# Performance work log

Hardware: AMD Instinct MI355X
Metric: run time of the kernel (lower is better)

## Reference

```python
import jax, jax.numpy as jnp
import numpy as np

NEG_INF = -1.0e12  # matches masked_fill value in the torch module


def _entmax15(x, axis=-1):
    """Exact entmax with alpha=1.5 (Peters & Martins, 2019), sort-based."""
    x = x - jnp.max(x, axis=axis, keepdims=True)
    x = x / 2.0
    d = x.shape[axis]
    xs = -jnp.sort(-x, axis=axis)  # descending sort along normalization axis
    rho = jnp.arange(1, d + 1, dtype=x.dtype)  # 1..d, broadcasts on last axis
    mean = jnp.cumsum(xs, axis=axis) / rho
    mean_sq = jnp.cumsum(xs * xs, axis=axis) / rho
    ss = rho * (mean_sq - mean * mean)
    delta = (1.0 - ss) / rho
    tau = mean - jnp.sqrt(jnp.clip(delta, 0.0))
    support = jnp.sum((tau <= xs).astype(jnp.int32), axis=axis, keepdims=True)
    tau_star = jnp.take_along_axis(tau, support - 1, axis=axis)
    y = jnp.clip(x - tau_star, 0.0)
    return y * y


def setup_inputs() -> dict:
    key = jax.random.key(0)
    kq, kk, kv, km = jax.random.split(key, 4)
    B, H, S, D = 4, 8, 1024, 128
    q = jax.random.normal(kq, (B, H, S, D), dtype=jnp.float32)
    k = jax.random.normal(kk, (B, H, S, D), dtype=jnp.float32)
    v = jax.random.normal(kv, (B, H, S, D), dtype=jnp.float32)
    mask = jax.random.randint(km, (B, 1, S, S), 0, 2, dtype=jnp.int32)
    return {"q": q, "k": k, "v": v, "mask": mask}


def reference(q, k, v, mask):
    D = q.shape[-1]
    scale = 1.0 / jnp.sqrt(jnp.asarray(D, dtype=q.dtype))
    scores = jnp.einsum("bhqd,bhkd->bhqk", q, k) * scale
    scores = jnp.where(mask == 0, jnp.asarray(NEG_INF, dtype=scores.dtype), scores)
    attn = _entmax15(scores, axis=-1)
    return jnp.einsum("bhqk,bhkd->bhqd", attn, v)
```

## Files before the change

### kernel.cpp

```cpp
#include <hip/hip_runtime.h>


#define S_ 1024
#define D_ 128
#define NEG_INF_F (-1.0e12f)
#define SCALE_F 0.08838834764831845f
#define NITER 14

typedef float f32x4 __attribute__((ext_vector_type(4)));
typedef short short8 __attribute__((ext_vector_type(8)));

__device__ __forceinline__ ushort f2bf(float x) {
    unsigned u = __builtin_bit_cast(unsigned, x);
    u += 0x7FFFu + ((u >> 16) & 1u);
    return (ushort)(u >> 16);
}
__device__ __forceinline__ float bf2f(ushort h) {
    unsigned u = ((unsigned)h) << 16;
    return __builtin_bit_cast(float, u);
}
__device__ __forceinline__ short8 cvt8(float4 a, float4 b) {
    short8 r; ushort* p = (ushort*)&r;
    p[0] = f2bf(a.x); p[1] = f2bf(a.y); p[2] = f2bf(a.z); p[3] = f2bf(a.w);
    p[4] = f2bf(b.x); p[5] = f2bf(b.y); p[6] = f2bf(b.z); p[7] = f2bf(b.w);
    return r;
}

__global__ __launch_bounds__(256)
void pre_cvt(const float* __restrict__ K, const float* __restrict__ V,
             ushort* __restrict__ Kb, ushort* __restrict__ Vt)
{
    __shared__ __align__(16) ushort tileT[64][68];
    const int t = threadIdx.x;
    if (blockIdx.x < 4096) {
        int i = blockIdx.x * 256 + t;
        float4 v = ((const float4*)K)[i];
        ushort4 o;
        o.x = f2bf(v.x); o.y = f2bf(v.y); o.z = f2bf(v.z); o.w = f2bf(v.w);
        ((ushort4*)Kb)[i] = o;
        return;
    }
    const int vb = blockIdx.x - 4096;
    const int bh = vb >> 5, r5 = vb & 31, kt = r5 >> 1, dh = r5 & 1;
    const float* src = V + ((size_t)(bh * S_ + kt * 64)) * D_ + dh * 64;
    #pragma unroll
    for (int i = 0; i < 4; ++i) {
        int idx = t + i * 256, r = idx >> 4, c = idx & 15;
        float4 vv = *(const float4*)(src + (size_t)r * D_ + c * 4);
        tileT[c * 4 + 0][r] = f2bf(vv.x);
        tileT[c * 4 + 1][r] = f2bf(vv.y);
        tileT[c * 4 + 2][r] = f2bf(vv.z);
        tileT[c * 4 + 3][r] = f2bf(vv.w);
    }
    __syncthreads();
    ushort* dst = Vt + ((size_t)(bh * D_ + dh * 64)) * S_ + kt * 64;
    #pragma unroll
    for (int i = 0; i < 2; ++i) {
        int idx = t + i * 256, d = idx >> 3, jj = idx & 7;
        short8 val = *(const short8*)&tileT[d][jj * 8];
        *(short8*)(dst + (size_t)d * S_ + jj * 8) = val;
    }
}

__global__ __launch_bounds__(512, 3)
void entmax_attn(const float* __restrict__ Q, const ushort* __restrict__ Kb,
                 const ushort* __restrict__ Vt, const int* __restrict__ M,
                 float* __restrict__ O)
{
    __shared__ __align__(16) ushort sc[16][1024];

    const int t = threadIdx.x;
    const int w = t >> 6, lane = t & 63, l = lane & 15, quad = lane >> 4;
    const int swz = (blockIdx.x & 7) * 256 + (blockIdx.x >> 3);
    const int bh = swz >> 6, qt = swz & 63, b = bh >> 3;

    const ushort* kb_bh = Kb + (size_t)bh * (S_ * D_);
    const ushort* vt_bh = Vt + (size_t)bh * (D_ * S_);

    short8 aq[4];
    {
        const float* qr = Q + ((size_t)(bh * S_ + qt * 16 + l)) * D_ + quad * 8;
        #pragma unroll
        for (int ks = 0; ks < 4; ++ks) {
            float4 qa = *(const float4*)(qr + ks * 32);
            float4 qb = *(const float4*)(qr + ks * 32 + 4);
            aq[ks] = cvt8(qa, qb);
        }
    }

    const ushort* kp = kb_bh + (size_t)(w * 16 + l) * D_ + quad * 8;
    short8 c0 = *(const short8*)(kp +  0);
    short8 c1 = *(const short8*)(kp + 32);
    short8 c2 = *(const short8*)(kp + 64);
    short8 c3 = *(const short8*)(kp + 96);

    #pragma unroll 1
    for (int kt = 0; kt < 7; ++kt) {
        const ushort* np = kp + (size_t)(kt + 1) * (128 * D_);
        short8 n0 = *(const short8*)(np +  0);
        short8 n1 = *(const short8*)(np + 32);
        short8 n2 = *(const short8*)(np + 64);
        short8 n3 = *(const short8*)(np + 96);
        f32x4 acc = {0.f, 0.f, 0.f, 0.f};
        __builtin_amdgcn_s_setprio(1);
        acc = __builtin_amdgcn_mfma_f32_16x16x32_bf16(aq[0], c0, acc, 0, 0, 0);
        acc = __builtin_amdgcn_mfma_f32_16x16x32_bf16(aq[1], c1, acc, 0, 0, 0);
        acc = __builtin_amdgcn_mfma_f32_16x16x32_bf16(aq[2], c2, acc, 0, 0, 0);
        acc = __builtin_amdgcn_mfma_f32_16x16x32_bf16(aq[3], c3, acc, 0, 0, 0);
        __builtin_amdgcn_s_setprio(0);
        const int coln = kt * 16 + w * 2 + (l >> 3);
        #pragma unroll
        for (int r = 0; r < 4; ++r) {
            const int rr = quad * 4 + r;
            sc[rr][((coln ^ (rr & 7)) << 3) + (l & 7)] = f2bf(acc[r] * SCALE_F);
        }
        c0 = n0; c1 = n1; c2 = n2; c3 = n3;
    }
    {
        f32x4 acc = {0.f, 0.f, 0.f, 0.f};
        __builtin_amdgcn_s_setprio(1);
        acc = __builtin_amdgcn_mfma_f32_16x16x32_bf16(aq[0], c0, acc, 0, 0, 0);
        acc = __builtin_amdgcn_mfma_f32_16x16x32_bf16(aq[1], c1, acc, 0, 0, 0);
        acc = __builtin_amdgcn_mfma_f32_16x16x32_bf16(aq[2], c2, acc, 0, 0, 0);
        acc = __builtin_amdgcn_mfma_f32_16x16x32_bf16(aq[3], c3, acc, 0, 0, 0);
        __builtin_amdgcn_s_setprio(0);
        const int coln = 7 * 16 + w * 2 + (l >> 3);
        #pragma unroll
        for (int r = 0; r < 4; ++r) {
            const int rr = quad * 4 + r;
            sc[rr][((coln ^ (rr & 7)) << 3) + (l & 7)] = f2bf(acc[r] * SCALE_F);
        }
    }
    __syncthreads();

    const int row = t >> 5, u = t & 31;
    const int qg = qt * 16 + row;
    float x[32];
    #pragma unroll
    for (int c = 0; c < 4; ++c) {
        short8 v8 = *(const short8*)&sc[row][((c * 32 + u) ^ (row & 7)) << 3];
        #pragma unroll
        for (int e = 0; e < 8; ++e) x[c * 8 + e] = bf2f(((ushort*)&v8)[e]);
    }
    {
        const int4* mrow = (const int4*)(M + ((size_t)b * S_ + qg) * S_);
        #pragma unroll
        for (int c = 0; c < 4; ++c) {
            #pragma unroll
            for (int h = 0; h < 2; ++h) {
                int4 mm = mrow[c * 64 + u * 2 + h];
                if (mm.x == 0) x[c * 8 + h * 4 + 0] = NEG_INF_F;
                if (mm.y == 0) x[c * 8 + h * 4 + 1] = NEG_INF_F;
                if (mm.z == 0) x[c * 8 + h * 4 + 2] = NEG_INF_F;
                if (mm.w == 0) x[c * 8 + h * 4 + 3] = NEG_INF_F;
            }
        }
    }
    float mx = -3.0e38f;
    #pragma unroll
    for (int j = 0; j < 32; ++j) mx = fmaxf(mx, x[j]);
    #pragma unroll
    for (int off = 1; off < 32; off <<= 1) mx = fmaxf(mx, __shfl_xor(mx, off));
    #pragma unroll
    for (int j = 0; j < 32; ++j) x[j] = (x[j] - mx) * 0.5f;

    float lo = -1.f, hi = 0.f;
    #pragma unroll 1
    for (int it = 0; it < NITER; ++it) {
        const float tm = 0.5f * (lo + hi);
        float f = 0.f;
        #pragma unroll
        for (int j = 0; j < 32; ++j) {
            float d = fmaxf(x[j] - tm, 0.f);
            f = fmaf(d, d, f);
        }
        #pragma unroll
        for (int off = 1; off < 32; off <<= 1) f += __shfl_xor(f, off);
        const bool ge = (f >= 1.f);
        lo = ge ? tm : lo;
        hi = ge ? hi : tm;
    }
    const float tau = 0.5f * (lo + hi);

    #pragma unroll
    for (int c = 0; c < 4; ++c) {
        short8 v8;
        #pragma unroll
        for (int e = 0; e < 8; ++e) {
            float d = fmaxf(x[c * 8 + e] - tau, 0.f);
            ((ushort*)&v8)[e] = f2bf(d * d);
        }
        *(short8*)&sc[row][((c * 32 + u) ^ (row & 7)) << 3] = v8;
    }

    const ushort* vp = vt_bh + (size_t)(w * 16 + l) * S_ + quad * 8;
    short8 v0 = *(const short8*)(vp +  0);
    short8 v1 = *(const short8*)(vp + 32);
    short8 v2 = *(const short8*)(vp + 64);
    short8 v3 = *(const short8*)(vp + 96);
    __syncthreads();

    f32x4 oa = {0.f, 0.f, 0.f, 0.f};
    #pragma unroll 1
    for (int vt = 0; vt < 7; ++vt) {
        const ushort* np = vp + (size_t)(vt + 1) * 128;
        short8 n0 = *(const short8*)(np +  0);
        short8 n1 = *(const short8*)(np + 32);
        short8 n2 = *(const short8*)(np + 64);
        short8 n3 = *(const short8*)(np + 96);
        short8 a0 = *(const short8*)&sc[l][((vt * 16 +  0 + quad) ^ (l & 7)) << 3];
        short8 a1 = *(const short8*)&sc[l][((vt * 16 +  4 + quad) ^ (l & 7)) << 3];
        short8 a2 = *(const short8*)&sc[l][((vt * 16 +  8 + quad) ^ (l & 7)) << 3];
        short8 a3 = *(const short8*)&sc[l][((vt * 16 + 12 + quad) ^ (l & 7)) << 3];
        __builtin_amdgcn_s_setprio(1);
        oa = __builtin_amdgcn_mfma_f32_16x16x32_bf16(a0, v0, oa, 0, 0, 0);
        oa = __builtin_amdgcn_mfma_f32_16x16x32_bf16(a1, v1, oa, 0, 0, 0);
        oa = __builtin_amdgcn_mfma_f32_16x16x32_bf16(a2, v2, oa, 0, 0, 0);
        oa = __builtin_amdgcn_mfma_f32_16x16x32_bf16(a3, v3, oa, 0, 0, 0);
        __builtin_amdgcn_s_setprio(0);
        v0 = n0; v1 = n1; v2 = n2; v3 = n3;
    }
    {
        short8 a0 = *(const short8*)&sc[l][((7 * 16 +  0 + quad) ^ (l & 7)) << 3];
        short8 a1 = *(const short8*)&sc[l][((7 * 16 +  4 + quad) ^ (l & 7)) << 3];
        short8 a2 = *(const short8*)&sc[l][((7 * 16 +  8 + quad) ^ (l & 7)) << 3];
        short8 a3 = *(const short8*)&sc[l][((7 * 16 + 12 + quad) ^ (l & 7)) << 3];
        __builtin_amdgcn_s_setprio(1);
        oa = __builtin_amdgcn_mfma_f32_16x16x32_bf16(a0, v0, oa, 0, 0, 0);
        oa = __builtin_amdgcn_mfma_f32_16x16x32_bf16(a1, v1, oa, 0, 0, 0);
        oa = __builtin_amdgcn_mfma_f32_16x16x32_bf16(a2, v2, oa, 0, 0, 0);
        oa = __builtin_amdgcn_mfma_f32_16x16x32_bf16(a3, v3, oa, 0, 0, 0);
        __builtin_amdgcn_s_setprio(0);
    }

    float* ob = O + ((size_t)bh * S_ + (size_t)qt * 16) * D_;
    #pragma unroll
    for (int r = 0; r < 4; ++r)
        ob[(size_t)(quad * 4 + r) * D_ + w * 16 + l] = oa[r];
}

extern "C" void kernel_launch(void* const* d_in, const int* in_sizes, int n_in,
                              void* d_out, int out_size, void* d_ws, size_t ws_size,
                              hipStream_t stream) {
    const float* q = (const float*)d_in[0];
    const float* k = (const float*)d_in[1];
    const float* v = (const float*)d_in[2];
    const int*   m = (const int*)d_in[3];
    float*       o = (float*)d_out;

    ushort* Kb = (ushort*)d_ws;
    ushort* Vt = (ushort*)((char*)d_ws + 8388608);

    pre_cvt<<<5120, 256, 0, stream>>>(k, v, Kb, Vt);
    entmax_attn<<<2048, 512, 0, stream>>>(q, Kb, Vt, m, o);
}
```

Baseline: 234.9 us.

## Bit-pack mask in preprocessing and bisect entmax threshold over compacted candidates

The pre-conversion kernel gains extra blocks that pack the int32 mask into 32-bit bitmasks. Before, the attention kernel re-read the full int32 mask row for every head; now it loads one packed word per thread. The entmax bisection now first compacts the scores above -1 into a shared-memory candidate list, since only those can lie in the support. It then bisects over that list, falling back to the full register scan if there are more than 512 candidates. The V operand loads are also hoisted before the first barrier, and the PV MFMAs are interleaved with LDS reads. This adds ballot/prefix work and a data-dependent loop in exchange for less mask traffic and fewer bisection FLOPs.

Measured after the change: 248.6 us. +5.8%, slower.

```diff
diff --git a/kernel.cpp b/kernel.cpp
--- a/kernel.cpp
+++ b/kernel.cpp
@@ -6,6 +6,7 @@
 #define NEG_INF_F (-1.0e12f)
 #define SCALE_F 0.08838834764831845f
 #define NITER 14
+#define CCAP 512
 
 typedef float f32x4 __attribute__((ext_vector_type(4)));
 typedef short short8 __attribute__((ext_vector_type(8)));
@@ -28,7 +29,9 @@
 
 __global__ __launch_bounds__(256)
 void pre_cvt(const float* __restrict__ K, const float* __restrict__ V,
-             ushort* __restrict__ Kb, ushort* __restrict__ Vt)
+             const int* __restrict__ M,
+             ushort* __restrict__ Kb, ushort* __restrict__ Vt,
+             unsigned* __restrict__ Mp)
 {
     __shared__ __align__(16) ushort tileT[64][68];
     const int t = threadIdx.x;
@@ -40,6 +43,25 @@
         ((ushort4*)Kb)[i] = o;
         return;
     }
+    if (blockIdx.x >= 5120) {
+        const int g = (blockIdx.x - 5120) * 256 + t;
+        const int mrow = g >> 5, u = g & 31;
+        const int* src = M + (size_t)mrow * 1024 + u * 8;
+        unsigned out = 0;
+        #pragma unroll
+        for (int c = 0; c < 4; ++c) {
+            int4 a = *(const int4*)(src + c * 256);
+            int4 b4 = *(const int4*)(src + c * 256 + 4);
+            unsigned byte =
+                (unsigned)(a.x != 0)       | ((unsigned)(a.y != 0) << 1) |
+                ((unsigned)(a.z != 0) << 2)| ((unsigned)(a.w != 0) << 3) |
+                ((unsigned)(b4.x != 0) << 4)| ((unsigned)(b4.y != 0) << 5) |
+                ((unsigned)(b4.z != 0) << 6)| ((unsigned)(b4.w != 0) << 7);
+            out |= byte << (c * 8);
+        }
+        Mp[(size_t)mrow * 32 + u] = out;
+        return;
+    }
     const int vb = blockIdx.x - 4096;
     const int bh = vb >> 5, r5 = vb & 31, kt = r5 >> 1, dh = r5 & 1;
     const float* src = V + ((size_t)(bh * S_ + kt * 64)) * D_ + dh * 64;
@@ -64,7 +86,7 @@
 
 __global__ __launch_bounds__(512, 3)
 void entmax_attn(const float* __restrict__ Q, const ushort* __restrict__ Kb,
-                 const ushort* __restrict__ Vt, const int* __restrict__ M,
+                 const ushort* __restrict__ Vt, const unsigned* __restrict__ Mp,
                  float* __restrict__ O)
 {
     __shared__ __align__(16) ushort sc[16][1024];
@@ -76,6 +98,10 @@
 
     const ushort* kb_bh = Kb + (size_t)bh * (S_ * D_);
     const ushort* vt_bh = Vt + (size_t)bh * (D_ * S_);
+
+    const int row = t >> 5, u = t & 31;
+    const int qg = qt * 16 + row;
+    const unsigned mw = Mp[(size_t)(b * S_ + qg) * 32 + u];
 
     short8 aq[4];
     {
@@ -131,10 +157,13 @@
             sc[rr][((coln ^ (rr & 7)) << 3) + (l & 7)] = f2bf(acc[r] * SCALE_F);
         }
     }
+    const ushort* vp = vt_bh + (size_t)(w * 16 + l) * S_ + quad * 8;
+    c0 = *(const short8*)(vp +  0);
+    c1 = *(const short8*)(vp + 32);
+    c2 = *(const short8*)(vp + 64);
+    c3 = *(const short8*)(vp + 96);
     __syncthreads();
 
-    const int row = t >> 5, u = t & 31;
-    const int qg = qt * 16 + row;
     float x[32];
     #pragma unroll
     for (int c = 0; c < 4; ++c) {
@@ -142,45 +171,74 @@
         #pragma unroll
         for (int e = 0; e < 8; ++e) x[c * 8 + e] = bf2f(((ushort*)&v8)[e]);
     }
-    {
-        const int4* mrow = (const int4*)(M + ((size_t)b * S_ + qg) * S_);
-        #pragma unroll
-        for (int c = 0; c < 4; ++c) {
+    #pragma unroll
+    for (int c = 0; c < 4; ++c) {
+        #pragma unroll
+        for (int e = 0; e < 8; ++e)
+            if (!((mw >> (c * 8 + e)) & 1u)) x[c * 8 + e] = NEG_INF_F;
+    }
+    float mx = -3.0e38f;
+    #pragma unroll
+    for (int j = 0; j < 32; ++j) mx = fmaxf(mx, x[j]);
+    #pragma unroll
+    for (int off = 1; off < 32; off <<= 1) mx = fmaxf(mx, __shfl_xor(mx, off));
+    #pragma unroll
+    for (int j = 0; j < 32; ++j) x[j] = (x[j] - mx) * 0.5f;
+
+    float* cand = (float*)&sc[row][0];
+    const unsigned long long halfmask =
+        (lane >= 32) ? 0xFFFFFFFF00000000ull : 0x00000000FFFFFFFFull;
+    int cnt = 0;
+    #pragma unroll
+    for (int j = 0; j < 32; ++j) {
+        const bool p = (x[j] > -1.0f);
+        unsigned long long bal = __ballot(p) & halfmask;
+        if (p) {
+            int pos = cnt + (int)__builtin_amdgcn_mbcnt_hi(
+                (unsigned)(bal >> 32),
+                __builtin_amdgcn_mbcnt_lo((unsigned)bal, 0));
+            if (pos < CCAP) cand[pos] = x[j];
+        }
+        cnt += __popcll(bal);
+    }
+
+    float tau;
+    if (cnt <= CCAP) {
+        float lo = -1.f, hi = 0.f;
+        #pragma unroll 1
+        for (int it = 0; it < NITER; ++it) {
+            const float tm = 0.5f * (lo + hi);
+            float f = 0.f;
+            for (int j = u; j < cnt; j += 32) {
+                float d = fmaxf(cand[j] - tm, 0.f);
+                f = fmaf(d, d, f);
+            }
             #pragma unroll
-            for (int h = 0; h < 2; ++h) {
-                int4 mm = mrow[c * 64 + u * 2 + h];
-                if (mm.x == 0) x[c * 8 + h * 4 + 0] = NEG_INF_F;
-                if (mm.y == 0) x[c * 8 + h * 4 + 1] = NEG_INF_F;
-                if (mm.z == 0) x[c * 8 + h * 4 + 2] = NEG_INF_F;
-                if (mm.w == 0) x[c * 8 + h * 4 + 3] = NEG_INF_F;
+            for (int off = 1; off < 32; off <<= 1) f += __shfl_xor(f, off);
+            const bool ge = (f >= 1.f);
+            lo = ge ? tm : lo;
+            hi = ge ? hi : tm;
+        }
+        tau = 0.5f * (lo + hi);
+    } else {
+        float lo = -1.f, hi = 0.f;
+        #pragma unroll 1
+        for (int it = 0; it < NITER; ++it) {
+            const float tm = 0.5f * (lo + hi);
+            float f = 0.f;
+            #pragma unroll
+            for (int j = 0; j < 32; ++j) {
+                float d = fmaxf(x[j] - tm, 0.f);
+                f = fmaf(d, d, f);
             }
-        }
-    }
-    float mx = -3.0e38f;
-    #pragma unroll
-    for (int j = 0; j < 32; ++j) mx = fmaxf(mx, x[j]);
-    #pragma unroll
-    for (int off = 1; off < 32; off <<= 1) mx = fmaxf(mx, __shfl_xor(mx, off));
-    #pragma unroll
-    for (int j = 0; j < 32; ++j) x[j] = (x[j] - mx) * 0.5f;
-
-    float lo = -1.f, hi = 0.f;
-    #pragma unroll 1
-    for (int it = 0; it < NITER; ++it) {
-        const float tm = 0.5f * (lo + hi);
-        float f = 0.f;
-        #pragma unroll
-        for (int j = 0; j < 32; ++j) {
-            float d = fmaxf(x[j] - tm, 0.f);
-            f = fmaf(d, d, f);
-        }
-        #pragma unroll
-        for (int off = 1; off < 32; off <<= 1) f += __shfl_xor(f, off);
-        const bool ge = (f >= 1.f);
-        lo = ge ? tm : lo;
-        hi = ge ? hi : tm;
-    }
-    const float tau = 0.5f * (lo + hi);
+            #pragma unroll
+            for (int off = 1; off < 32; off <<= 1) f += __shfl_xor(f, off);
+            const bool ge = (f >= 1.f);
+            lo = ge ? tm : lo;
+            hi = ge ? hi : tm;
+        }
+        tau = 0.5f * (lo + hi);
+    }
 
     #pragma unroll
     for (int c = 0; c < 4; ++c) {
@@ -192,12 +250,6 @@
         }
         *(short8*)&sc[row][((c * 32 + u) ^ (row & 7)) << 3] = v8;
     }
-
-    const ushort* vp = vt_bh + (size_t)(w * 16 + l) * S_ + quad * 8;
-    short8 v0 = *(const short8*)(vp +  0);
-    short8 v1 = *(const short8*)(vp + 32);
-    short8 v2 = *(const short8*)(vp + 64);
-    short8 v3 = *(const short8*)(vp + 96);
     __syncthreads();
 
     f32x4 oa = {0.f, 0.f, 0.f, 0.f};
@@ -210,15 +262,17 @@
         short8 n3 = *(const short8*)(np + 96);
         short8 a0 = *(const short8*)&sc[l][((vt * 16 +  0 + quad) ^ (l & 7)) << 3];
         short8 a1 = *(const short8*)&sc[l][((vt * 16 +  4 + quad) ^ (l & 7)) << 3];
+        __builtin_amdgcn_s_setprio(1);
+        oa = __builtin_amdgcn_mfma_f32_16x16x32_bf16(a0, c0, oa, 0, 0, 0);
+        oa = __builtin_amdgcn_mfma_f32_16x16x32_bf16(a1, c1, oa, 0, 0, 0);
+        __builtin_amdgcn_s_setprio(0);
         short8 a2 = *(const short8*)&sc[l][((vt * 16 +  8 + quad) ^ (l & 7)) << 3];
         short8 a3 = *(const short8*)&sc[l][((vt * 16 + 12 + quad) ^ (l & 7)) << 3];
         __builtin_amdgcn_s_setprio(1);
-        oa = __builtin_amdgcn_mfma_f32_16x16x32_bf16(a0, v0, oa, 0, 0, 0);
-        oa = __builtin_amdgcn_mfma_f32_16x16x32_bf16(a1, v1, oa, 0, 0, 0);
-        oa = __builtin_amdgcn_mfma_f32_16x16x32_bf16(a2, v2, oa, 0, 0, 0);
-        oa = __builtin_amdgcn_mfma_f32_16x16x32_bf16(a3, v3, oa, 0, 0, 0);
-        __builtin_amdgcn_s_setprio(0);
-        v0 = n0; v1 = n1; v2 = n2; v3 = n3;
+        oa = __builtin_amdgcn_mfma_f32_16x16x32_bf16(a2, c2, oa, 0, 0, 0);
+        oa = __builtin_amdgcn_mfma_f32_16x16x32_bf16(a3, c3, oa, 0, 0, 0);
+        __builtin_amdgcn_s_setprio(0);
+        c0 = n0; c1 = n1; c2 = n2; c3 = n3;
     }
     {
         short8 a0 = *(const short8*)&sc[l][((7 * 16 +  0 + quad) ^ (l & 7)) << 3];
@@ -226,10 +280,10 @@
         short8 a2 = *(const short8*)&sc[l][((7 * 16 +  8 + quad) ^ (l & 7)) << 3];
         short8 a3 = *(const short8*)&sc[l][((7 * 16 + 12 + quad) ^ (l & 7)) << 3];
         __builtin_amdgcn_s_setprio(1);
-        oa = __builtin_amdgcn_mfma_f32_16x16x32_bf16(a0, v0, oa, 0, 0, 0);
-        oa = __builtin_amdgcn_mfma_f32_16x16x32_bf16(a1, v1, oa, 0, 0, 0);
-        oa = __builtin_amdgcn_mfma_f32_16x16x32_bf16(a2, v2, oa, 0, 0, 0);
-        oa = __builtin_amdgcn_mfma_f32_16x16x32_bf16(a3, v3, oa, 0, 0, 0);
+        oa = __builtin_amdgcn_mfma_f32_16x16x32_bf16(a0, c0, oa, 0, 0, 0);
+        oa = __builtin_amdgcn_mfma_f32_16x16x32_bf16(a1, c1, oa, 0, 0, 0);
+        oa = __builtin_amdgcn_mfma_f32_16x16x32_bf16(a2, c2, oa, 0, 0, 0);
+        oa = __builtin_amdgcn_mfma_f32_16x16x32_bf16(a3, c3, oa, 0, 0, 0);
         __builtin_amdgcn_s_setprio(0);
     }
 
@@ -248,9 +302,10 @@
     const int*   m = (const int*)d_in[3];
     float*       o = (float*)d_out;
 
-    ushort* Kb = (ushort*)d_ws;
-    ushort* Vt = (ushort*)((char*)d_ws + 8388608);
-
-    pre_cvt<<<5120, 256, 0, stream>>>(k, v, Kb, Vt);
-    entmax_attn<<<2048, 512, 0, stream>>>(q, Kb, Vt, m, o);
-}
+    ushort*   Kb = (ushort*)d_ws;
+    ushort*   Vt = (ushort*)((char*)d_ws + 8388608);
+    unsigned* Mp = (unsigned*)((char*)d_ws + 16777216);
+
+    pre_cvt<<<5632, 256, 0, stream>>>(k, v, m, Kb, Vt, Mp);
+    entmax_attn<<<2048, 512, 0, stream>>>(q, Kb, Vt, Mp, o);
+}
```
